# Kernel optimization log

Measured on AMD Instinct MI355X. Metric: run time of the kernel, lower is better.

## Reference

```python
import jax, jax.numpy as jnp
import numpy as np

N = 100000
D = 128
E = 600000


def setup_inputs() -> dict:
    key = jax.random.key(0)
    k = jax.random.split(key, 7)
    x = jax.random.normal(k[0], (N, D), dtype=jnp.float32)
    edge_index = jax.random.randint(k[1], (2, E), 0, N, dtype=jnp.int32)
    edge_weight = jax.random.uniform(k[2], (E,), dtype=jnp.float32)
    # Linear params (torch nn.Linear: y = x @ W.T + b), init scale ~ 1/sqrt(D)
    s = 1.0 / np.sqrt(D)
    W1 = jax.random.uniform(k[3], (D, D), minval=-s, maxval=s, dtype=jnp.float32)
    b1 = jax.random.uniform(k[4], (D,), minval=-s, maxval=s, dtype=jnp.float32)
    W2 = jax.random.uniform(k[5], (D, D), minval=-s, maxval=s, dtype=jnp.float32)
    b2 = jax.random.uniform(k[6], (D,), minval=-s, maxval=s, dtype=jnp.float32)
    return {"x": x, "edge_index": edge_index, "edge_weight": edge_weight,
            "W1": W1, "b1": b1, "W2": W2, "b2": b2}


def reference(x, edge_index, edge_weight, W1, b1, W2, b2):
    row, col = edge_index[0], edge_index[1]
    # gather-weight-scatter: agg[col] += w * x[row]
    msgs = edge_weight[:, None] * x[row]            # [E, D]
    agg = jax.ops.segment_sum(msgs, col, num_segments=x.shape[0])  # [N, D]
    h = (agg + x) @ W1.T + b1 + (agg * x) @ W2.T + b2
    out = jax.nn.leaky_relu(h, negative_slope=0.2)
    # dropout omitted (eval-mode reference)
    return out
```

## Files before the change

### kernel.cpp

```cpp
#include <hip/hip_runtime.h>

#define D 128

typedef __attribute__((ext_vector_type(8))) short short8;
typedef __attribute__((ext_vector_type(4))) float f32x4;

__device__ __forceinline__ unsigned int f2bf(float f) {
  unsigned int u = __float_as_uint(f);
  return (u + 0x7fffu + ((u >> 16) & 1u)) >> 16;
}

__global__ __launch_bounds__(256) void prep_k(
    const float* __restrict__ W1, const float* __restrict__ b1,
    const float* __restrict__ W2, const float* __restrict__ b2,
    unsigned short* __restrict__ Bpack, float* __restrict__ bsum) {
  int tid = blockIdx.x * 256 + threadIdx.x;
  if (tid < 32768) {
    int j = tid & 7;
    int l = (tid >> 3) & 63;
    int ktnt = tid >> 9;
    int kt = ktnt >> 3, nt = ktnt & 7;
    int k = kt * 32 + ((l >> 4) << 3) + j;
    int col = nt * 16 + (l & 15);
    float v = (k < 128) ? W1[col * 128 + k] : W2[col * 128 + (k - 128)];
    Bpack[tid] = (unsigned short)f2bf(v);
  }
  if (tid < 128) bsum[tid] = b1[tid] + b2[tid];
}

__global__ __launch_bounds__(256) void hist_k(
    const int* __restrict__ ei, int* __restrict__ cursor, int E) {
  int e = blockIdx.x * 256 + threadIdx.x;
  if (e < E) atomicAdd(&cursor[ei[E + e]], 1);
}

__global__ __launch_bounds__(256) void scan_block_k(
    const int* __restrict__ deg, int* __restrict__ rowptr,
    int* __restrict__ partials, int Nn) {
  __shared__ int sdata[256];
  int t = threadIdx.x;
  int base = blockIdx.x * 1024 + t * 4;
  int v[4];
  #pragma unroll
  for (int j = 0; j < 4; ++j) v[j] = (base + j < Nn) ? deg[base + j] : 0;
  int tsum = v[0] + v[1] + v[2] + v[3];
  sdata[t] = tsum;
  __syncthreads();
  for (int off = 1; off < 256; off <<= 1) {
    int add = (t >= off) ? sdata[t - off] : 0;
    __syncthreads();
    sdata[t] += add;
    __syncthreads();
  }
  int run = sdata[t] - tsum;
  if (t == 255) partials[blockIdx.x] = sdata[255];
  #pragma unroll
  for (int j = 0; j < 4; ++j) {
    if (base + j < Nn) rowptr[base + j] = run;
    run += v[j];
  }
}

__global__ __launch_bounds__(128) void scan_partials_k(int* partials, int NB) {
  __shared__ int s[128];
  int t = threadIdx.x;
  int orig = (t < NB) ? partials[t] : 0;
  s[t] = orig;
  __syncthreads();
  for (int off = 1; off < 128; off <<= 1) {
    int add = (t >= off) ? s[t - off] : 0;
    __syncthreads();
    s[t] += add;
    __syncthreads();
  }
  if (t < NB) partials[t] = s[t] - orig;
}

__global__ __launch_bounds__(256) void add_offsets_k(
    int* __restrict__ rowptr, int* __restrict__ cursor,
    const int* __restrict__ partials, int Nn, int E) {
  int i = blockIdx.x * 256 + threadIdx.x;
  if (i < Nn) {
    int v = rowptr[i] + partials[i >> 10];
    rowptr[i] = v;
    cursor[i] = v;
  }
  if (i == 0) rowptr[Nn] = E;
}

__global__ __launch_bounds__(256) void fill_k(
    const int* __restrict__ ei, const float* __restrict__ ew,
    int* __restrict__ cursor, int2* __restrict__ edges, int E) {
  int e = blockIdx.x * 256 + threadIdx.x;
  if (e >= E) return;
  int c = ei[E + e];
  int p = atomicAdd(&cursor[c], 1);
  edges[p] = make_int2(ei[e], __float_as_int(ew[e]));
}

__global__ __launch_bounds__(256) void xbf_k(
    const float* __restrict__ x, unsigned short* __restrict__ xbf, int n8) {
  int tid = blockIdx.x * 256 + threadIdx.x;
  if (tid >= n8) return;
  float4 a = ((const float4*)x)[(size_t)tid * 2];
  float4 b = ((const float4*)x)[(size_t)tid * 2 + 1];
  uint4 o;
  o.x = f2bf(a.x) | (f2bf(a.y) << 16);
  o.y = f2bf(a.z) | (f2bf(a.w) << 16);
  o.z = f2bf(b.x) | (f2bf(b.y) << 16);
  o.w = f2bf(b.z) | (f2bf(b.w) << 16);
  ((uint4*)xbf)[tid] = o;
}

__global__ __launch_bounds__(256) void agg_k(
    const unsigned short* __restrict__ xbf, const int* __restrict__ rowptr,
    const int2* __restrict__ edges, float* __restrict__ agg, int Nn) {
  int node = blockIdx.x * 4 + (threadIdx.x >> 6);
  if (node >= Nn) return;
  int l = threadIdx.x & 63;
  int half = l >> 5, sl = l & 31;
  int beg = rowptr[node], end = rowptr[node + 1];
  float4 acc = make_float4(0.f, 0.f, 0.f, 0.f);
  for (int p = beg + half; p < end; p += 8) {
    int2 e[4];
    #pragma unroll
    for (int i = 0; i < 4; ++i) e[i] = edges[min(p + 2 * i, end - 1)];
    uint2 v[4];
    #pragma unroll
    for (int i = 0; i < 4; ++i)
      v[i] = *(const uint2*)(xbf + (size_t)e[i].x * D + sl * 4);
    #pragma unroll
    for (int i = 0; i < 4; ++i) {
      float w = (p + 2 * i < end) ? __int_as_float(e[i].y) : 0.f;
      acc.x += w * __uint_as_float(v[i].x << 16);
      acc.y += w * __uint_as_float(v[i].x & 0xffff0000u);
      acc.z += w * __uint_as_float(v[i].y << 16);
      acc.w += w * __uint_as_float(v[i].y & 0xffff0000u);
    }
  }
  acc.x += __shfl_xor(acc.x, 32);
  acc.y += __shfl_xor(acc.y, 32);
  acc.z += __shfl_xor(acc.z, 32);
  acc.w += __shfl_xor(acc.w, 32);
  if (half == 0)
    ((float4*)(agg + (size_t)node * D))[sl] = acc;
}

__global__ __launch_bounds__(256, 4) void fused_k(
    const float* __restrict__ x, const float* __restrict__ agg,
    const unsigned short* __restrict__ Bpack, const float* __restrict__ bsum,
    float* __restrict__ out, int Nn) {
  constexpr int ROWB = 528;
  __shared__ __align__(16) unsigned char Us[64 * ROWB];
  const int t = threadIdx.x;
  const int node0 = blockIdx.x * 64;

  #pragma unroll
  for (int i = 0; i < 8; ++i) {
    int f4 = t + i * 256;
    int node = f4 >> 5;
    int d4 = f4 & 31;
    int g = node0 + node;
    float4 a4 = make_float4(0.f, 0.f, 0.f, 0.f), x4 = a4;
    if (g < Nn) {
      a4 = ((const float4*)agg)[(size_t)g * 32 + d4];
      x4 = ((const float4*)x)[(size_t)g * 32 + d4];
    }
    uint2 up, vp;
    up.x = f2bf(a4.x + x4.x) | (f2bf(a4.y + x4.y) << 16);
    up.y = f2bf(a4.z + x4.z) | (f2bf(a4.w + x4.w) << 16);
    vp.x = f2bf(a4.x * x4.x) | (f2bf(a4.y * x4.y) << 16);
    vp.y = f2bf(a4.z * x4.z) | (f2bf(a4.w * x4.w) << 16);
    *(uint2*)(Us + node * ROWB + d4 * 8)       = up;
    *(uint2*)(Us + node * ROWB + 256 + d4 * 8) = vp;
  }
  __syncthreads();

  const int lane = t & 63, w = t >> 6;
  const int c15 = lane & 15, kq = lane >> 4;

  short8 afr[8];
  const unsigned char* abase = Us + (size_t)(w * 16 + c15) * ROWB + kq * 16;
  #pragma unroll
  for (int kt = 0; kt < 8; ++kt)
    afr[kt] = *(const short8*)(abase + kt * 64);

  f32x4 acc[8];
  #pragma unroll
  for (int nt = 0; nt < 8; ++nt) acc[nt] = (f32x4){0.f, 0.f, 0.f, 0.f};

  const short8* bp = (const short8*)Bpack + lane;
  #pragma unroll
  for (int kt = 0; kt < 8; ++kt) {
    #pragma unroll
    for (int nt = 0; nt < 8; ++nt) {
      short8 bfr = bp[(kt * 8 + nt) * 64];
      acc[nt] = __builtin_amdgcn_mfma_f32_16x16x32_bf16(afr[kt], bfr, acc[nt], 0, 0, 0);
    }
  }

  float bsv[8];
  #pragma unroll
  for (int nt = 0; nt < 8; ++nt) bsv[nt] = bsum[nt * 16 + c15];

  #pragma unroll
  for (int r = 0; r < 4; ++r) {
    int g = node0 + w * 16 + kq * 4 + r;
    if (g >= Nn) continue;
    float* orow = out + (size_t)g * D + c15;
    #pragma unroll
    for (int nt = 0; nt < 8; ++nt) {
      float h = acc[nt][r] + bsv[nt];
      orow[nt * 16] = h > 0.f ? h : 0.2f * h;
    }
  }
}

extern "C" void kernel_launch(void* const* d_in, const int* in_sizes, int n_in,
                              void* d_out, int out_size, void* d_ws, size_t ws_size,
                              hipStream_t stream) {
  const float* x  = (const float*)d_in[0];
  const int*   ei = (const int*)d_in[1];
  const float* ew = (const float*)d_in[2];
  const float* W1 = (const float*)d_in[3];
  const float* b1 = (const float*)d_in[4];
  const float* W2 = (const float*)d_in[5];
  const float* b2 = (const float*)d_in[6];
  float* out = (float*)d_out;

  const int Nn = in_sizes[0] / D;
  const int E  = in_sizes[2];
  const int NB = (Nn + 1023) / 1024;

  const size_t xbfB    = (((size_t)Nn * D * 2) + 255) & ~(size_t)255;
  const size_t edgesB  = (size_t)E * sizeof(int2);
  const size_t cursorB = (((size_t)Nn * 4) + 255) & ~(size_t)255;
  const size_t rowptrB = (((size_t)(Nn + 1) * 4) + 255) & ~(size_t)255;
  const size_t partB   = 1024;
  const size_t BpackB  = 65536;
  const size_t bsB     = 512;
  const size_t aggB    = (size_t)Nn * D * sizeof(float);

  char* base = (char*)d_ws;
  unsigned short* xbf   = (unsigned short*)base;  base += xbfB;
  int2*  edges   = (int2*)base;                   base += edgesB;
  int*   cursor  = (int*)base;                    base += cursorB;
  int*   rowptr  = (int*)base;                    base += rowptrB;
  int*   partials= (int*)base;                    base += partB;
  unsigned short* Bpack = (unsigned short*)base;  base += BpackB;
  float* bs      = (float*)base;                  base += bsB;
  size_t used = (size_t)(base - (char*)d_ws);
  float* agg = (ws_size >= used + aggB) ? (float*)base : out;

  hipMemsetAsync(cursor, 0, (size_t)Nn * 4, stream);
  int eBlocks = (E + 255) / 256;
  hist_k<<<eBlocks, 256, 0, stream>>>(ei, cursor, E);
  scan_block_k<<<NB, 256, 0, stream>>>(cursor, rowptr, partials, Nn);
  scan_partials_k<<<1, 128, 0, stream>>>(partials, NB);
  add_offsets_k<<<(Nn + 255) / 256, 256, 0, stream>>>(rowptr, cursor, partials, Nn, E);
  fill_k<<<eBlocks, 256, 0, stream>>>(ei, ew, cursor, edges, E);

  prep_k<<<128, 256, 0, stream>>>(W1, b1, W2, b2, Bpack, bs);

  int n8 = Nn * D / 8;
  xbf_k<<<(n8 + 255) / 256, 256, 0, stream>>>(x, xbf, n8);

  agg_k<<<(Nn + 3) / 4, 256, 0, stream>>>(xbf, rowptr, edges, agg, Nn);

  fused_k<<<(Nn + 63) / 64, 256, 0, stream>>>(x, agg, Bpack, bs, out, Nn);
}
```

Measured before the change: 249.5 us.

## Fuse aggregation into GEMM kernel and merge small preprocessing launches

Moves the gather-weight-scatter aggregation into the fused GEMM kernel: each wave computes agg for its 16 nodes directly into shared memory, so the fp32 agg buffer is never written to or read back from global memory. The xbf conversion is merged with the histogram kernel, and the weight-packing kernel is merged with add_offsets, which cuts the number of launches. As a trade-off, the aggregation now runs inside a kernel limited to 4 blocks by launch bounds with large LDS use. Each wave walks its nodes one after another with one 4-byte load per lane, so load imbalance and reduced memory-level parallelism in the gather could hurt.

```diff
diff --git a/kernel.cpp b/kernel.cpp
--- a/kernel.cpp
+++ b/kernel.cpp
@@ -10,28 +10,25 @@
   return (u + 0x7fffu + ((u >> 16) & 1u)) >> 16;
 }
 
-__global__ __launch_bounds__(256) void prep_k(
-    const float* __restrict__ W1, const float* __restrict__ b1,
-    const float* __restrict__ W2, const float* __restrict__ b2,
-    unsigned short* __restrict__ Bpack, float* __restrict__ bsum) {
-  int tid = blockIdx.x * 256 + threadIdx.x;
-  if (tid < 32768) {
-    int j = tid & 7;
-    int l = (tid >> 3) & 63;
-    int ktnt = tid >> 9;
-    int kt = ktnt >> 3, nt = ktnt & 7;
-    int k = kt * 32 + ((l >> 4) << 3) + j;
-    int col = nt * 16 + (l & 15);
-    float v = (k < 128) ? W1[col * 128 + k] : W2[col * 128 + (k - 128)];
-    Bpack[tid] = (unsigned short)f2bf(v);
-  }
-  if (tid < 128) bsum[tid] = b1[tid] + b2[tid];
-}
-
-__global__ __launch_bounds__(256) void hist_k(
-    const int* __restrict__ ei, int* __restrict__ cursor, int E) {
-  int e = blockIdx.x * 256 + threadIdx.x;
-  if (e < E) atomicAdd(&cursor[ei[E + e]], 1);
+__global__ __launch_bounds__(256) void pre1_k(
+    const float* __restrict__ x, unsigned short* __restrict__ xbf, int n8,
+    const int* __restrict__ ei, int* __restrict__ cursor, int E, int XB) {
+  int b = blockIdx.x;
+  if (b < XB) {
+    int tid = b * 256 + threadIdx.x;
+    if (tid >= n8) return;
+    float4 a = ((const float4*)x)[(size_t)tid * 2];
+    float4 c = ((const float4*)x)[(size_t)tid * 2 + 1];
+    uint4 o;
+    o.x = f2bf(a.x) | (f2bf(a.y) << 16);
+    o.y = f2bf(a.z) | (f2bf(a.w) << 16);
+    o.z = f2bf(c.x) | (f2bf(c.y) << 16);
+    o.w = f2bf(c.z) | (f2bf(c.w) << 16);
+    ((uint4*)xbf)[tid] = o;
+  } else {
+    int e = (b - XB) * 256 + threadIdx.x;
+    if (e < E) atomicAdd(&cursor[ei[E + e]], 1);
+  }
 }
 
 __global__ __launch_bounds__(256) void scan_block_k(
@@ -76,16 +73,36 @@
   if (t < NB) partials[t] = s[t] - orig;
 }
 
-__global__ __launch_bounds__(256) void add_offsets_k(
+__global__ __launch_bounds__(256) void addoff_prep_k(
     int* __restrict__ rowptr, int* __restrict__ cursor,
-    const int* __restrict__ partials, int Nn, int E) {
-  int i = blockIdx.x * 256 + threadIdx.x;
-  if (i < Nn) {
-    int v = rowptr[i] + partials[i >> 10];
-    rowptr[i] = v;
-    cursor[i] = v;
-  }
-  if (i == 0) rowptr[Nn] = E;
+    const int* __restrict__ partials,
+    const float* __restrict__ W1, const float* __restrict__ b1,
+    const float* __restrict__ W2, const float* __restrict__ b2,
+    unsigned short* __restrict__ Bpack, float* __restrict__ bsum,
+    int Nn, int E, int AB) {
+  int b = blockIdx.x;
+  if (b < AB) {
+    int i = b * 256 + threadIdx.x;
+    if (i < Nn) {
+      int v = rowptr[i] + partials[i >> 10];
+      rowptr[i] = v;
+      cursor[i] = v;
+    }
+    if (i == 0) rowptr[Nn] = E;
+  } else {
+    int tid = (b - AB) * 256 + threadIdx.x;
+    if (tid < 32768) {
+      int j = tid & 7;
+      int l = (tid >> 3) & 63;
+      int ktnt = tid >> 9;
+      int kt = ktnt >> 3, nt = ktnt & 7;
+      int k = kt * 32 + ((l >> 4) << 3) + j;
+      int col = nt * 16 + (l & 15);
+      float v = (k < 128) ? W1[col * 128 + k] : W2[col * 128 + (k - 128)];
+      Bpack[tid] = (unsigned short)f2bf(v);
+    }
+    if (tid < 128) bsum[tid] = b1[tid] + b2[tid];
+  }
 }
 
 __global__ __launch_bounds__(256) void fill_k(
@@ -98,85 +115,48 @@
   edges[p] = make_int2(ei[e], __float_as_int(ew[e]));
 }
 
-__global__ __launch_bounds__(256) void xbf_k(
-    const float* __restrict__ x, unsigned short* __restrict__ xbf, int n8) {
-  int tid = blockIdx.x * 256 + threadIdx.x;
-  if (tid >= n8) return;
-  float4 a = ((const float4*)x)[(size_t)tid * 2];
-  float4 b = ((const float4*)x)[(size_t)tid * 2 + 1];
-  uint4 o;
-  o.x = f2bf(a.x) | (f2bf(a.y) << 16);
-  o.y = f2bf(a.z) | (f2bf(a.w) << 16);
-  o.z = f2bf(b.x) | (f2bf(b.y) << 16);
-  o.w = f2bf(b.z) | (f2bf(b.w) << 16);
-  ((uint4*)xbf)[tid] = o;
-}
-
-__global__ __launch_bounds__(256) void agg_k(
-    const unsigned short* __restrict__ xbf, const int* __restrict__ rowptr,
-    const int2* __restrict__ edges, float* __restrict__ agg, int Nn) {
-  int node = blockIdx.x * 4 + (threadIdx.x >> 6);
-  if (node >= Nn) return;
-  int l = threadIdx.x & 63;
-  int half = l >> 5, sl = l & 31;
-  int beg = rowptr[node], end = rowptr[node + 1];
-  float4 acc = make_float4(0.f, 0.f, 0.f, 0.f);
-  for (int p = beg + half; p < end; p += 8) {
-    int2 e[4];
-    #pragma unroll
-    for (int i = 0; i < 4; ++i) e[i] = edges[min(p + 2 * i, end - 1)];
-    uint2 v[4];
-    #pragma unroll
-    for (int i = 0; i < 4; ++i)
-      v[i] = *(const uint2*)(xbf + (size_t)e[i].x * D + sl * 4);
-    #pragma unroll
-    for (int i = 0; i < 4; ++i) {
-      float w = (p + 2 * i < end) ? __int_as_float(e[i].y) : 0.f;
-      acc.x += w * __uint_as_float(v[i].x << 16);
-      acc.y += w * __uint_as_float(v[i].x & 0xffff0000u);
-      acc.z += w * __uint_as_float(v[i].y << 16);
-      acc.w += w * __uint_as_float(v[i].y & 0xffff0000u);
-    }
-  }
-  acc.x += __shfl_xor(acc.x, 32);
-  acc.y += __shfl_xor(acc.y, 32);
-  acc.z += __shfl_xor(acc.z, 32);
-  acc.w += __shfl_xor(acc.w, 32);
-  if (half == 0)
-    ((float4*)(agg + (size_t)node * D))[sl] = acc;
-}
-
-__global__ __launch_bounds__(256, 4) void fused_k(
-    const float* __restrict__ x, const float* __restrict__ agg,
+__global__ __launch_bounds__(256, 4) void aggfused_k(
+    const unsigned short* __restrict__ xbf, const float* __restrict__ x,
+    const int* __restrict__ rowptr, const int2* __restrict__ edges,
     const unsigned short* __restrict__ Bpack, const float* __restrict__ bsum,
     float* __restrict__ out, int Nn) {
   constexpr int ROWB = 528;
   __shared__ __align__(16) unsigned char Us[64 * ROWB];
   const int t = threadIdx.x;
   const int node0 = blockIdx.x * 64;
-
-  #pragma unroll
-  for (int i = 0; i < 8; ++i) {
-    int f4 = t + i * 256;
-    int node = f4 >> 5;
-    int d4 = f4 & 31;
+  const int lane = t & 63, w = t >> 6;
+
+  for (int i = 0; i < 16; ++i) {
+    int node = w * 16 + i;
     int g = node0 + node;
-    float4 a4 = make_float4(0.f, 0.f, 0.f, 0.f), x4 = a4;
+    uint up = 0, vp = 0;
     if (g < Nn) {
-      a4 = ((const float4*)agg)[(size_t)g * 32 + d4];
-      x4 = ((const float4*)x)[(size_t)g * 32 + d4];
-    }
-    uint2 up, vp;
-    up.x = f2bf(a4.x + x4.x) | (f2bf(a4.y + x4.y) << 16);
-    up.y = f2bf(a4.z + x4.z) | (f2bf(a4.w + x4.w) << 16);
-    vp.x = f2bf(a4.x * x4.x) | (f2bf(a4.y * x4.y) << 16);
-    vp.y = f2bf(a4.z * x4.z) | (f2bf(a4.w * x4.w) << 16);
-    *(uint2*)(Us + node * ROWB + d4 * 8)       = up;
-    *(uint2*)(Us + node * ROWB + 256 + d4 * 8) = vp;
+      float ax = 0.f, ay = 0.f;
+      int beg = rowptr[g], end = rowptr[g + 1];
+      for (int p = beg; p < end; p += 8) {
+        int2 e[8];
+        #pragma unroll
+        for (int q = 0; q < 8; ++q) e[q] = edges[min(p + q, end - 1)];
+        unsigned int v[8];
+        #pragma unroll
+        for (int q = 0; q < 8; ++q)
+          v[q] = *(const unsigned int*)(xbf + (size_t)e[q].x * D + lane * 2);
+        #pragma unroll
+        for (int q = 0; q < 8; ++q) {
+          float wt = (p + q < end) ? __int_as_float(e[q].y) : 0.f;
+          ax += wt * __uint_as_float(v[q] << 16);
+          ay += wt * __uint_as_float(v[q] & 0xffff0000u);
+        }
+      }
+      float2 xr = *(const float2*)(x + (size_t)g * D + lane * 2);
+      up = f2bf(ax + xr.x) | (f2bf(ay + xr.y) << 16);
+      vp = f2bf(ax * xr.x) | (f2bf(ay * xr.y) << 16);
+    }
+    *(unsigned int*)(Us + node * ROWB + lane * 4)       = up;
+    *(unsigned int*)(Us + node * ROWB + 256 + lane * 4) = vp;
   }
   __syncthreads();
 
-  const int lane = t & 63, w = t >> 6;
   const int c15 = lane & 15, kq = lane >> 4;
 
   short8 afr[8];
@@ -238,8 +218,6 @@
   const size_t rowptrB = (((size_t)(Nn + 1) * 4) + 255) & ~(size_t)255;
   const size_t partB   = 1024;
   const size_t BpackB  = 65536;
-  const size_t bsB     = 512;
-  const size_t aggB    = (size_t)Nn * D * sizeof(float);
 
   char* base = (char*)d_ws;
   unsigned short* xbf   = (unsigned short*)base;  base += xbfB;
@@ -248,24 +226,25 @@
   int*   rowptr  = (int*)base;                    base += rowptrB;
   int*   partials= (int*)base;                    base += partB;
   unsigned short* Bpack = (unsigned short*)base;  base += BpackB;
-  float* bs      = (float*)base;                  base += bsB;
-  size_t used = (size_t)(base - (char*)d_ws);
-  float* agg = (ws_size >= used + aggB) ? (float*)base : out;
+  float* bs      = (float*)base;
 
   hipMemsetAsync(cursor, 0, (size_t)Nn * 4, stream);
-  int eBlocks = (E + 255) / 256;
-  hist_k<<<eBlocks, 256, 0, stream>>>(ei, cursor, E);
+
+  const int n8 = Nn * D / 8;
+  const int XB = (n8 + 255) / 256;
+  const int HB = (E + 255) / 256;
+  pre1_k<<<XB + HB, 256, 0, stream>>>(x, xbf, n8, ei, cursor, E, XB);
+
   scan_block_k<<<NB, 256, 0, stream>>>(cursor, rowptr, partials, Nn);
   scan_partials_k<<<1, 128, 0, stream>>>(partials, NB);
-  add_offsets_k<<<(Nn + 255) / 256, 256, 0, stream>>>(rowptr, cursor, partials, Nn, E);
-  fill_k<<<eBlocks, 256, 0, stream>>>(ei, ew, cursor, edges, E);
-
-  prep_k<<<128, 256, 0, stream>>>(W1, b1, W2, b2, Bpack, bs);
-
-  int n8 = Nn * D / 8;
-  xbf_k<<<(n8 + 255) / 256, 256, 0, stream>>>(x, xbf, n8);
-
-  agg_k<<<(Nn + 3) / 4, 256, 0, stream>>>(xbf, rowptr, edges, agg, Nn);
-
-  fused_k<<<(Nn + 63) / 64, 256, 0, stream>>>(x, agg, Bpack, bs, out, Nn);
-}
+
+  const int AB = (Nn + 255) / 256;
+  addoff_prep_k<<<AB + 128, 256, 0, stream>>>(rowptr, cursor, partials,
+                                              W1, b1, W2, b2, Bpack, bs,
+                                              Nn, E, AB);
+
+  fill_k<<<HB, 256, 0, stream>>>(ei, ew, cursor, edges, E);
+
+  aggfused_k<<<(Nn + 63) / 64, 256, 0, stream>>>(xbf, x, rowptr, edges,
+                                                 Bpack, bs, out, Nn);
+}
```

New measurement: 253.8 us. No clear change (+1.7%).
